# Kernel optimization log

Hardware: AMD Instinct MI355X
Metric: run time of the kernel (lower is better)

The kernel has to match this reference:

```python
import jax, jax.numpy as jnp
import numpy as np

BLANK = 0
FASTEMIT_LAMBDA = 1e-3


def setup_inputs() -> dict:
    key = jax.random.key(0)
    B, T, U, V = 8, 256, 65, 1024
    k1, k2, k3, k4 = jax.random.split(key, 4)
    acts = jax.random.normal(k1, (B, T, U, V), dtype=jnp.float32)
    # labels in [1, V) (blank=0 excluded), zero-padded semantics irrelevant since we gather by length
    labels = jax.random.randint(k2, (B, U - 1), 1, V, dtype=jnp.int32)
    # lengths: first example pinned to max so max(act_lens)==T and max(label_lens)==U-1
    act_lens = jnp.concatenate([
        jnp.array([T], dtype=jnp.int32),
        jax.random.randint(k3, (B - 1,), T // 2, T + 1, dtype=jnp.int32),
    ])
    label_lens = jnp.concatenate([
        jnp.array([U - 1], dtype=jnp.int32),
        jax.random.randint(k4, (B - 1,), (U - 1) // 2, U, dtype=jnp.int32),
    ])
    return {"acts": acts, "labels": labels, "act_lens": act_lens, "label_lens": label_lens}


def _rnnt_loss(acts, labels, act_lens, label_lens):
    B, T, U, V = acts.shape
    lp = jax.nn.log_softmax(acts, axis=-1)            # (B,T,U,V)
    lp_blank = lp[..., BLANK]                          # (B,T,U)
    # lp_label[b,t,u] = lp[b,t,u,labels[b,u]], u in [0, U-1)
    lp_label = jnp.take_along_axis(
        lp[:, :, : U - 1, :],
        jnp.broadcast_to(labels[:, None, :, None].astype(jnp.int32), (B, T, U - 1, 1)),
        axis=-1,
    )[..., 0]                                          # (B,T,U-1)
    # FastEmit: scale only the *gradient* of label-emission log-probs by (1+lambda);
    # forward value unchanged (matches warp-transducer fastemit grad formulation).
    lam = jnp.float32(FASTEMIT_LAMBDA)
    lp_label = (1.0 + lam) * lp_label - lam * jax.lax.stop_gradient(lp_label)

    def u_scan(b_row, label_row):
        # alpha_t[u] = logaddexp(b_row[u], alpha_t[u-1] + label_row[u-1]); sequential in u
        a0 = b_row[:, 0]                               # (B,)
        def step(carry, xs):
            b_u, c_u = xs
            a = jnp.logaddexp(b_u, carry + c_u)
            return a, a
        _, rest = jax.lax.scan(step, a0, (b_row[:, 1:].T, label_row.T))  # (U-1,B)
        return jnp.concatenate([a0[None], rest], axis=0).T               # (B,U)

    # t = 0 row: only label moves -> cumulative sum of label log-probs
    alpha0 = jnp.concatenate(
        [jnp.zeros((B, 1), acts.dtype), jnp.cumsum(lp_label[:, 0, :], axis=1)], axis=1
    )                                                  # (B,U)

    def t_step(alpha_prev, xs):
        lpb_prev, lpl_t = xs                           # (B,U), (B,U-1)
        b_row = alpha_prev + lpb_prev                  # blank transition from t-1
        alpha_t = u_scan(b_row, lpl_t)
        return alpha_t, alpha_t

    xs = (jnp.swapaxes(lp_blank[:, :-1, :], 0, 1),     # (T-1,B,U)
          jnp.swapaxes(lp_label[:, 1:, :], 0, 1))      # (T-1,B,U-1)
    _, alphas_rest = jax.lax.scan(t_step, alpha0, xs)  # (T-1,B,U)
    alphas = jnp.concatenate([alpha0[None], alphas_rest], axis=0)  # (T,B,U)

    bidx = jnp.arange(B)
    t_idx = act_lens.astype(jnp.int32) - 1
    u_idx = label_lens.astype(jnp.int32)
    ll = alphas[t_idx, bidx, u_idx] + lp_blank[bidx, t_idx, u_idx]  # final blank emission
    costs = -ll
    # reduction == 'mean': sum then divide by minibatch size, shape (1,)
    return (jnp.sum(costs) / B)[None]


def reference(acts, labels, act_lens, label_lens):
    return _rnnt_loss(acts, labels, act_lens, label_lens)
```

## Files before the change

kernel.cpp:

```cpp
#include <hip/hip_runtime.h>
#include <hip/hip_bf16.h>

#define B_ 8
#define T_ 256
#define U_ 65
#define V_ 1024
#define DIAGS (T_ + U_ - 1)
#define DSTRIDE (DIAGS * U_)
#define PF 8

__device__ __forceinline__ float laddexp(float x, float y) {
  float m = fmaxf(x, y);
  return m + __logf(1.0f + __expf(-fabsf(x - y)));
}

__global__ __launch_bounds__(256) void rnnt_lse_kernel(
    const float* __restrict__ acts, const int* __restrict__ labels,
    float* __restrict__ blankD, float* __restrict__ labelD) {
  const int wave = threadIdx.x >> 6;
  const int lane = threadIdx.x & 63;
  const int row = blockIdx.x * 4 + wave;

  const float* __restrict__ p = acts + (size_t)row * V_;
  const float4* __restrict__ p4 = (const float4*)p;
  float4 v0 = p4[lane];
  float4 v1 = p4[64 + lane];
  float4 v2 = p4[128 + lane];
  float4 v3 = p4[192 + lane];

  float m = fmaxf(fmaxf(fmaxf(v0.x, v0.y), fmaxf(v0.z, v0.w)),
                  fmaxf(fmaxf(v1.x, v1.y), fmaxf(v1.z, v1.w)));
  m = fmaxf(m, fmaxf(fmaxf(fmaxf(v2.x, v2.y), fmaxf(v2.z, v2.w)),
                     fmaxf(fmaxf(v3.x, v3.y), fmaxf(v3.z, v3.w))));
  #pragma unroll
  for (int off = 32; off; off >>= 1) m = fmaxf(m, __shfl_xor(m, off, 64));

  float s = (__expf(v0.x - m) + __expf(v0.y - m)) +
            (__expf(v0.z - m) + __expf(v0.w - m));
  s += (__expf(v1.x - m) + __expf(v1.y - m)) +
       (__expf(v1.z - m) + __expf(v1.w - m));
  s += (__expf(v2.x - m) + __expf(v2.y - m)) +
       (__expf(v2.z - m) + __expf(v2.w - m));
  s += (__expf(v3.x - m) + __expf(v3.y - m)) +
       (__expf(v3.z - m) + __expf(v3.w - m));
  #pragma unroll
  for (int off = 32; off; off >>= 1) s += __shfl_xor(s, off, 64);

  float lse = m + __logf(s);

  if (lane == 0) {
    const int b = row / (T_ * U_);
    const int rem = row - b * (T_ * U_);
    const int t = rem / U_;
    const int u = rem - t * U_;
    blankD[b * DSTRIDE + (t + u) * U_ + u] = v0.x - lse;
    if (u < U_ - 1) {
      const int lab = labels[b * (U_ - 1) + u];
      labelD[b * DSTRIDE + (t + u + 1) * U_ + (u + 1)] = p[lab] - lse;
    }
  }
}

__global__ __launch_bounds__(512) void rnnt_alpha_kernel(
    const float* __restrict__ blankD, const float* __restrict__ labelD,
    const int* __restrict__ act_lens, const int* __restrict__ label_lens,
    float* __restrict__ out) {
  const int wv = threadIdx.x >> 6;
  const int lane = threadIdx.x & 63;
  const float* __restrict__ BD = blankD + wv * DSTRIDE;
  const float* __restrict__ LD = labelD + wv * DSTRIDE;

  const int t_end = act_lens[wv] - 1;
  const int u_end = label_lens[wv];
  const int d_end = t_end + u_end;
  const bool use64 = (u_end == 64);

  float a = 0.f;
  float a64 = 0.f;
  float cap = 0.f;

  float bdb[PF], ldb[PF], bdb64[PF], ldb64[PF];
  #pragma unroll
  for (int j = 0; j < PF; ++j) {
    const int rb = (j >= 1) ? (j - 1) : 0;
    bdb[j] = BD[rb * U_ + lane];
    ldb[j] = LD[j * U_ + lane];
    bdb64[j] = BD[rb * U_ + 64];
    ldb64[j] = LD[j * U_ + 64];
  }

  for (int d = 0; d <= d_end; d += PF) {
    #pragma unroll
    for (int j = 0; j < PF; ++j) {
      const int dd = d + j;
      const float am1 = __shfl_up(a, 1, 64);
      const float pa = a;
      const float pa64 = a64;
      const float bd = bdb[j];
      const float ld = ldb[j];

      const int t = dd - lane;
      if (t >= 0 && t < T_) {
        float na;
        if (t == 0) {
          na = (lane == 0) ? 0.f : (am1 + ld);
        } else if (lane == 0) {
          na = pa + bd;
        } else {
          na = laddexp(pa + bd, am1 + ld);
        }
        a = na;
      }
      if (lane == 63) {
        const int t64 = dd - 64;
        if (t64 >= 0 && t64 < T_) {
          a64 = (t64 == 0) ? (pa + ldb64[j])
                           : laddexp(pa64 + bdb64[j], pa + ldb64[j]);
        }
      }
      if (dd == d_end) cap = use64 ? a64 : a;

      int rb2 = dd + PF - 1; if (rb2 >= DIAGS) rb2 = DIAGS - 1;
      int rl2 = dd + PF;     if (rl2 >= DIAGS) rl2 = DIAGS - 1;
      bdb[j] = BD[rb2 * U_ + lane];
      ldb[j] = LD[rl2 * U_ + lane];
      bdb64[j] = BD[rb2 * U_ + 64];
      ldb64[j] = LD[rl2 * U_ + 64];
    }
  }

  const int src = use64 ? 63 : u_end;
  const float alpha_end = __shfl(cap, src, 64);

  __shared__ float partial[B_];
  if (lane == 0) {
    partial[wv] = -(alpha_end + BD[d_end * U_ + u_end]) * (1.0f / B_);
  }
  __syncthreads();
  if (threadIdx.x == 0) {
    float s = 0.f;
    #pragma unroll
    for (int i = 0; i < B_; ++i) s += partial[i];
    out[0] = s;
  }
}

extern "C" void kernel_launch(void* const* d_in, const int* in_sizes, int n_in,
                              void* d_out, int out_size, void* d_ws, size_t ws_size,
                              hipStream_t stream) {
  const float* acts = (const float*)d_in[0];
  const int* labels = (const int*)d_in[1];
  const int* act_lens = (const int*)d_in[2];
  const int* label_lens = (const int*)d_in[3];
  float* out = (float*)d_out;

  float* blankD = (float*)d_ws;
  float* labelD = blankD + (size_t)B_ * DSTRIDE;

  const int rows = B_ * T_ * U_;
  rnnt_lse_kernel<<<rows / 4, 256, 0, stream>>>(acts, labels, blankD, labelD);
  rnnt_alpha_kernel<<<1, 512, 0, stream>>>(blankD, labelD, act_lens, label_lens, out);
}
```

Before: 748.7 us.

## Fuse log-softmax and alpha recursion into one kernel with sentinel-based spin waiting

```diff
diff --git a/kernel.cpp b/kernel.cpp
--- a/kernel.cpp
+++ b/kernel.cpp
@@ -8,65 +8,76 @@
 #define DIAGS (T_ + U_ - 1)
 #define DSTRIDE (DIAGS * U_)
 #define PF 8
+#define SENT 0xFFFFFFFFu
+
+__device__ __forceinline__ unsigned ld_agent(const float* p) {
+  return __hip_atomic_load((const unsigned*)p, __ATOMIC_RELAXED,
+                           __HIP_MEMORY_SCOPE_AGENT);
+}
+__device__ __forceinline__ void st_agent(float* p, float v) {
+  __hip_atomic_store((unsigned*)p, __float_as_uint(v), __ATOMIC_RELAXED,
+                     __HIP_MEMORY_SCOPE_AGENT);
+}
 
 __device__ __forceinline__ float laddexp(float x, float y) {
   float m = fmaxf(x, y);
   return m + __logf(1.0f + __expf(-fabsf(x - y)));
 }
 
-__global__ __launch_bounds__(256) void rnnt_lse_kernel(
+__global__ __launch_bounds__(512) void rnnt_fused_kernel(
     const float* __restrict__ acts, const int* __restrict__ labels,
-    float* __restrict__ blankD, float* __restrict__ labelD) {
-  const int wave = threadIdx.x >> 6;
-  const int lane = threadIdx.x & 63;
-  const int row = blockIdx.x * 4 + wave;
-
-  const float* __restrict__ p = acts + (size_t)row * V_;
-  const float4* __restrict__ p4 = (const float4*)p;
-  float4 v0 = p4[lane];
-  float4 v1 = p4[64 + lane];
-  float4 v2 = p4[128 + lane];
-  float4 v3 = p4[192 + lane];
-
-  float m = fmaxf(fmaxf(fmaxf(v0.x, v0.y), fmaxf(v0.z, v0.w)),
-                  fmaxf(fmaxf(v1.x, v1.y), fmaxf(v1.z, v1.w)));
-  m = fmaxf(m, fmaxf(fmaxf(fmaxf(v2.x, v2.y), fmaxf(v2.z, v2.w)),
-                     fmaxf(fmaxf(v3.x, v3.y), fmaxf(v3.z, v3.w))));
-  #pragma unroll
-  for (int off = 32; off; off >>= 1) m = fmaxf(m, __shfl_xor(m, off, 64));
-
-  float s = (__expf(v0.x - m) + __expf(v0.y - m)) +
-            (__expf(v0.z - m) + __expf(v0.w - m));
-  s += (__expf(v1.x - m) + __expf(v1.y - m)) +
-       (__expf(v1.z - m) + __expf(v1.w - m));
-  s += (__expf(v2.x - m) + __expf(v2.y - m)) +
-       (__expf(v2.z - m) + __expf(v2.w - m));
-  s += (__expf(v3.x - m) + __expf(v3.y - m)) +
-       (__expf(v3.z - m) + __expf(v3.w - m));
-  #pragma unroll
-  for (int off = 32; off; off >>= 1) s += __shfl_xor(s, off, 64);
-
-  float lse = m + __logf(s);
-
-  if (lane == 0) {
-    const int b = row / (T_ * U_);
-    const int rem = row - b * (T_ * U_);
-    const int t = rem / U_;
-    const int u = rem - t * U_;
-    blankD[b * DSTRIDE + (t + u) * U_ + u] = v0.x - lse;
-    if (u < U_ - 1) {
-      const int lab = labels[b * (U_ - 1) + u];
-      labelD[b * DSTRIDE + (t + u + 1) * U_ + (u + 1)] = p[lab] - lse;
-    }
-  }
-}
-
-__global__ __launch_bounds__(512) void rnnt_alpha_kernel(
-    const float* __restrict__ blankD, const float* __restrict__ labelD,
     const int* __restrict__ act_lens, const int* __restrict__ label_lens,
+    float* __restrict__ blankD, float* __restrict__ labelD,
     float* __restrict__ out) {
   const int wv = threadIdx.x >> 6;
   const int lane = threadIdx.x & 63;
+
+  if (blockIdx.x != 0) {
+    const int wg = (blockIdx.x - 1) * 8 + wv;
+    const int b = wg & 7;
+    const int r = wg >> 3;
+    const int t = r / U_;
+    const int u = r - t * U_;
+
+    const float* __restrict__ p =
+        acts + (((size_t)b * T_ + t) * U_ + u) * V_;
+    const float4* __restrict__ p4 = (const float4*)p;
+    float4 v0 = p4[lane];
+    float4 v1 = p4[64 + lane];
+    float4 v2 = p4[128 + lane];
+    float4 v3 = p4[192 + lane];
+
+    float m = fmaxf(fmaxf(fmaxf(v0.x, v0.y), fmaxf(v0.z, v0.w)),
+                    fmaxf(fmaxf(v1.x, v1.y), fmaxf(v1.z, v1.w)));
+    m = fmaxf(m, fmaxf(fmaxf(fmaxf(v2.x, v2.y), fmaxf(v2.z, v2.w)),
+                       fmaxf(fmaxf(v3.x, v3.y), fmaxf(v3.z, v3.w))));
+    #pragma unroll
+    for (int off = 32; off; off >>= 1) m = fmaxf(m, __shfl_xor(m, off, 64));
+
+    float s = (__expf(v0.x - m) + __expf(v0.y - m)) +
+              (__expf(v0.z - m) + __expf(v0.w - m));
+    s += (__expf(v1.x - m) + __expf(v1.y - m)) +
+         (__expf(v1.z - m) + __expf(v1.w - m));
+    s += (__expf(v2.x - m) + __expf(v2.y - m)) +
+         (__expf(v2.z - m) + __expf(v2.w - m));
+    s += (__expf(v3.x - m) + __expf(v3.y - m)) +
+         (__expf(v3.z - m) + __expf(v3.w - m));
+    #pragma unroll
+    for (int off = 32; off; off >>= 1) s += __shfl_xor(s, off, 64);
+
+    float lse = m + __logf(s);
+
+    if (lane == 0) {
+      st_agent(blankD + b * DSTRIDE + (t + u) * U_ + u, v0.x - lse);
+      if (u < U_ - 1) {
+        const int lab = labels[b * (U_ - 1) + u];
+        st_agent(labelD + b * DSTRIDE + (t + u + 1) * U_ + (u + 1),
+                 p[lab] - lse);
+      }
+    }
+    return;
+  }
+
   const float* __restrict__ BD = blankD + wv * DSTRIDE;
   const float* __restrict__ LD = labelD + wv * DSTRIDE;
 
@@ -79,27 +90,51 @@
   float a64 = 0.f;
   float cap = 0.f;
 
-  float bdb[PF], ldb[PF], bdb64[PF], ldb64[PF];
+  unsigned bdb[PF], ldb[PF], b64b[PF], l64b[PF];
   #pragma unroll
   for (int j = 0; j < PF; ++j) {
     const int rb = (j >= 1) ? (j - 1) : 0;
-    bdb[j] = BD[rb * U_ + lane];
-    ldb[j] = LD[j * U_ + lane];
-    bdb64[j] = BD[rb * U_ + 64];
-    ldb64[j] = LD[j * U_ + 64];
+    bdb[j] = ld_agent(BD + rb * U_ + lane);
+    ldb[j] = ld_agent(LD + j * U_ + lane);
+    b64b[j] = ld_agent(BD + rb * U_ + 64);
+    l64b[j] = ld_agent(LD + j * U_ + 64);
   }
 
   for (int d = 0; d <= d_end; d += PF) {
     #pragma unroll
     for (int j = 0; j < PF; ++j) {
       const int dd = d + j;
+      if (dd > d_end) break;
+
+      const int t = dd - lane;
+      const int t64 = dd - 64;
+      const bool need_bd = (t >= 1) && (t < T_);
+      const bool need_ld = (lane >= 1) && (t >= 0) && (t < T_);
+      const bool is63 = (lane == 63);
+      const bool need_b64 = is63 && (t64 >= 1) && (t64 < T_);
+      const bool need_l64 = is63 && (t64 >= 0) && (t64 < T_);
+
+      int guard = 0;
+      while (true) {
+        const bool ok = (!need_bd || bdb[j] != SENT) &&
+                        (!need_ld || ldb[j] != SENT) &&
+                        (!need_b64 || b64b[j] != SENT) &&
+                        (!need_l64 || l64b[j] != SENT);
+        if (__ballot(ok) == ~0ull) break;
+        if (++guard > 65536) break;
+        const int rb = (dd >= 1) ? (dd - 1) : 0;
+        bdb[j] = ld_agent(BD + rb * U_ + lane);
+        ldb[j] = ld_agent(LD + dd * U_ + lane);
+        b64b[j] = ld_agent(BD + rb * U_ + 64);
+        l64b[j] = ld_agent(LD + dd * U_ + 64);
+      }
+
       const float am1 = __shfl_up(a, 1, 64);
       const float pa = a;
       const float pa64 = a64;
-      const float bd = bdb[j];
-      const float ld = ldb[j];
-
-      const int t = dd - lane;
+      const float bd = __uint_as_float(bdb[j]);
+      const float ld = __uint_as_float(ldb[j]);
+
       if (t >= 0 && t < T_) {
         float na;
         if (t == 0) {
@@ -111,21 +146,21 @@
         }
         a = na;
       }
-      if (lane == 63) {
-        const int t64 = dd - 64;
-        if (t64 >= 0 && t64 < T_) {
-          a64 = (t64 == 0) ? (pa + ldb64[j])
-                           : laddexp(pa64 + bdb64[j], pa + ldb64[j]);
-        }
+      if (is63 && t64 >= 0 && t64 < T_) {
+        a64 = (t64 == 0)
+                  ? (pa + __uint_as_float(l64b[j]))
+                  : laddexp(pa64 + __uint_as_float(b64b[j]),
+                            pa + __uint_as_float(l64b[j]));
       }
       if (dd == d_end) cap = use64 ? a64 : a;
 
-      int rb2 = dd + PF - 1; if (rb2 >= DIAGS) rb2 = DIAGS - 1;
-      int rl2 = dd + PF;     if (rl2 >= DIAGS) rl2 = DIAGS - 1;
-      bdb[j] = BD[rb2 * U_ + lane];
-      ldb[j] = LD[rl2 * U_ + lane];
-      bdb64[j] = BD[rb2 * U_ + 64];
-      ldb64[j] = LD[rl2 * U_ + 64];
+      const int nd = dd + PF;
+      if (nd <= d_end) {
+        bdb[j] = ld_agent(BD + (nd - 1) * U_ + lane);
+        ldb[j] = ld_agent(LD + nd * U_ + lane);
+        b64b[j] = ld_agent(BD + (nd - 1) * U_ + 64);
+        l64b[j] = ld_agent(LD + nd * U_ + 64);
+      }
     }
   }
 
@@ -134,7 +169,12 @@
 
   __shared__ float partial[B_];
   if (lane == 0) {
-    partial[wv] = -(alpha_end + BD[d_end * U_ + u_end]) * (1.0f / B_);
+    unsigned fb;
+    int guard = 0;
+    do {
+      fb = ld_agent(BD + d_end * U_ + u_end);
+    } while (fb == SENT && ++guard < 1000000);
+    partial[wv] = -(alpha_end + __uint_as_float(fb)) * (1.0f / B_);
   }
   __syncthreads();
   if (threadIdx.x == 0) {
@@ -157,7 +197,8 @@
   float* blankD = (float*)d_ws;
   float* labelD = blankD + (size_t)B_ * DSTRIDE;
 
-  const int rows = B_ * T_ * U_;
-  rnnt_lse_kernel<<<rows / 4, 256, 0, stream>>>(acts, labels, blankD, labelD);
-  rnnt_alpha_kernel<<<1, 512, 0, stream>>>(blankD, labelD, act_lens, label_lens, out);
-}
+  hipMemsetAsync(d_ws, 0xFF, (size_t)2 * B_ * DSTRIDE * sizeof(float), stream);
+
+  rnnt_fused_kernel<<<1 + (B_ * T_ * U_) / 8, 512, 0, stream>>>(
+      acts, labels, act_lens, label_lens, blankD, labelD, out);
+}
```

Result: slower. 846.5 us (+13.1%).
